# Kernel tuning notes

Hardware: AMD Instinct MI355X
Metric: run time of the kernel (lower is better)

The kernel has to match this reference:

```python
import jax, jax.numpy as jnp
import numpy as np

NT, NS, NH, NG = 365, 1024, 64, 32
NW = NH * 8 + 2


def setup_inputs() -> dict:
    key = jax.random.key(0)
    k1, k2, k3, k4 = jax.random.split(key, 4)
    std = 1.0 / np.sqrt(NH)
    x = jax.random.normal(k1, (NT, NS, 4), dtype=jnp.float32)
    # make P (precip) nonnegative and T1 < T2 plausible-ish; math is still generic
    xc = jax.random.normal(k2, (NS, NG), dtype=jnp.float32)
    fc_w = jax.random.uniform(k3, (NW, NG), minval=-std, maxval=std, dtype=jnp.float32)
    fc_b = jax.random.uniform(k4, (NW,), minval=-std, maxval=std, dtype=jnp.float32)
    return {"x": x, "xc": xc, "fc_w": fc_w, "fc_b": fc_b}


def reference(x, xc, fc_w, fc_b):
    nh = NH
    P, E, T1, T2 = x[..., 0], x[..., 1], x[..., 2], x[..., 3]  # each [nt, ns]
    Ta = (T1 + T2) * 0.5
    # rain/snow partition: rP = 1 - arccos((T1+T2)/(T2-T1))/3.1415, masked
    valid = (T1 < 0) & (T2 > 0)
    denom = jnp.where(valid, T2 - T1, 1.0)
    ratio = jnp.clip(jnp.where(valid, (T1 + T2) / denom, 0.0), -0.999999, 0.999999)
    rP = 1.0 - jnp.arccos(ratio) / 3.1415
    rP = jnp.where(T1 >= 0, 1.0, rP)
    rP = jnp.where(T2 <= 0, 0.0, rP)
    Ps = (1.0 - rP) * P  # snow   [nt, ns]
    Pl = rP * P          # liquid [nt, ns]

    w = xc @ fc_w.T + fc_b  # [ns, nh*8+2]
    gm = jnp.exp(w[:, :nh]) + 1.0
    ge = jax.nn.sigmoid(w[:, nh:2 * nh]) * 2.0
    go = jax.nn.sigmoid(w[:, 2 * nh:3 * nh])
    gl = jnp.exp(w[:, 3 * nh:4 * nh] * 2.0)
    ga = jax.nn.softmax(w[:, 4 * nh:5 * nh], axis=1)  # Dropout in eval mode = identity
    gb = jax.nn.sigmoid(w[:, 5 * nh:6 * nh])
    qb = jax.nn.relu(w[:, -1]) / nh  # [ns]
    kb = jax.nn.sigmoid(w[:, 6 * nh:7 * nh]) / 10.0
    gi = jax.nn.sigmoid(w[:, 7 * nh:8 * nh])

    ns = P.shape[1]
    init = (jnp.zeros((ns, nh), jnp.float32),) * 3  # S0, H0, G0

    def step(carry, inp):
        S0, H0, G0 = carry
        Ps_k, Pl_k, Ta_k, E_k = inp  # each [ns]
        S = S0 + Ps_k[:, None]
        Sm = jnp.minimum(S0, jax.nn.relu(Ta_k[:, None] * gm))  # snowmelt
        H = jax.nn.relu(H0 + Sm + Pl_k[:, None] * gi - E_k[:, None] * ge)
        Q1 = jax.nn.relu(H - gl)
        Q2a = jnp.minimum(H, gl) * go
        Q2 = Q2a * (1.0 - gb)
        G = G0 + Q2a * gb
        Q3 = G * kb
        H0n = jnp.minimum(H - Q2a, gl)
        G0n = G - Q3
        S0n = S - Sm
        Y = jnp.sum((Q1 + Q2 + Q3 + qb[:, None]) * ga, axis=1)  # [ns]
        return (S0n, H0n, G0n), Y

    _, Yout = jax.lax.scan(step, init, (Ps, Pl, Ta, E))
    return Yout  # [nt, ns]
```

## Files before the change

### kernel.cpp

```cpp
#include <hip/hip_runtime.h>
#include <math.h>

#define NT_ 365
#define NS_ 1024
#define NH_ 64
#define NG_ 32
#define NW_ 514
#define CH_ 64
#define NCHUNK_ 6
#define YPAD_ 65
#define SUB_ 8

__device__ __forceinline__ float sigmoidf(float v) {
  return 1.0f / (1.0f + expf(-v));
}

__device__ __forceinline__ float4 compute_met(float4 xv) {
  const float P = xv.x, E = xv.y, T1 = xv.z, T2 = xv.w;
  const float Ta = (T1 + T2) * 0.5f;
  float rP;
  if (T2 <= 0.0f) {
    rP = 0.0f;
  } else if (T1 >= 0.0f) {
    rP = 1.0f;
  } else {
    float r = (T1 + T2) / (T2 - T1);
    r = fminf(fmaxf(r, -0.999999f), 0.999999f);
    rP = 1.0f - acosf(r) * (1.0f / 3.1415f);
  }
  float4 m;
  m.x = (1.0f - rP) * P;
  m.y = rP * P;
  m.z = fmaxf(Ta, 0.0f);
  m.w = E;
  return m;
}

__global__ __launch_bounds__(256) void waternet_scan(
    const float* __restrict__ x,
    const float* __restrict__ xc,
    const float* __restrict__ fc_w,
    const float* __restrict__ fc_b,
    float* __restrict__ out)
{
  __shared__ float4 smet[4][CH_];
  __shared__ float  ytile[4][CH_ * YPAD_];

  const int tid  = threadIdx.x;
  const int lane = tid & 63;
  const int wv   = tid >> 6;
  const int site = (blockIdx.x << 2) + wv;
  const int us   = __builtin_amdgcn_readfirstlane(site);
  const float4* xp = (const float4*)x;

  float4 xcur = xp[lane * NS_ + site];

  float acc[8];
#pragma unroll
  for (int k = 0; k < 8; ++k) acc[k] = fc_b[k * NH_ + lane];
  float accq = fc_b[NW_ - 1];

  const float4* xcq = (const float4*)(xc + us * NG_);
  const float4* wq4 = (const float4*)fc_w;
#pragma unroll
  for (int g4 = 0; g4 < NG_ / 4; ++g4) {
    const float4 xv = xcq[g4];
#pragma unroll
    for (int k = 0; k < 8; ++k) {
      const float4 w = wq4[(k * NH_ + lane) * (NG_ / 4) + g4];
      acc[k] = fmaf(xv.x, w.x, acc[k]);
      acc[k] = fmaf(xv.y, w.y, acc[k]);
      acc[k] = fmaf(xv.z, w.z, acc[k]);
      acc[k] = fmaf(xv.w, w.w, acc[k]);
    }
    {
      const float4 w = wq4[(NW_ - 1) * (NG_ / 4) + g4];
      accq = fmaf(xv.x, w.x, accq);
      accq = fmaf(xv.y, w.y, accq);
      accq = fmaf(xv.z, w.z, accq);
      accq = fmaf(xv.w, w.w, accq);
    }
  }

  const float gm = expf(acc[0]) + 1.0f;
  const float ge = sigmoidf(acc[1]) * 2.0f;
  const float go = sigmoidf(acc[2]);
  const float gl = expf(acc[3] * 2.0f);
  float mx = acc[4];
#pragma unroll
  for (int mm = 32; mm >= 1; mm >>= 1) mx = fmaxf(mx, __shfl_xor(mx, mm, 64));
  const float ex = expf(acc[4] - mx);
  float sm = ex;
#pragma unroll
  for (int mm = 32; mm >= 1; mm >>= 1) sm += __shfl_xor(sm, mm, 64);
  const float ga = ex / sm;
  const float gb = sigmoidf(acc[5]);
  const float kb = sigmoidf(acc[6]) * 0.1f;
  const float gi = sigmoidf(acc[7]);
  const float qb = fmaxf(accq, 0.0f) * (1.0f / NH_);
  const float kb1m = 1.0f - kb;
  const float nge  = -ge;
  const float gq1  = go * (1.0f - gb) - 1.0f;

  float S0 = 0.0f, H0 = 0.0f, G0 = 0.0f;

  smet[wv][lane] = compute_met(xcur);

  auto step = [&](const float4 mt, float* ywaddr) {
    const float melt = mt.z * gm;
    const float Sm   = fminf(S0, melt);
    const float base = H0 + Sm;
    S0 = (S0 - Sm) + mt.x;
    const float t3 = fmaf(mt.y, gi, base);
    const float H  = fmaxf(fmaf(mt.w, nge, t3), 0.0f);
    const float M  = fminf(H, gl);
    const float Q2a = M * go;
    H0 = fminf(H - Q2a, gl);
    const float G = fmaf(Q2a, gb, G0);
    G0 = G * kb1m;
    *ywaddr = fmaf(G, kb, fmaf(M, gq1, H)) * ga;
  };

  float*       yw = &ytile[wv][lane];
  const float* yr = &ytile[wv][lane * YPAD_];

#pragma unroll 1
  for (int c = 0; c < NCHUNK_; ++c) {
    int tn = (c + 1) * CH_ + lane;
    tn = (tn < NT_) ? tn : (NT_ - 1);
    const float4 xnext = xp[tn * NS_ + site];

    const float4* mp = &smet[wv][0];

    float4 mb0[SUB_], mb1[SUB_];
#pragma unroll
    for (int u = 0; u < SUB_; ++u) mb0[u] = mp[u];

#pragma unroll
    for (int sc = 0; sc < CH_ / SUB_; ++sc) {
      float4*       cur = (sc & 1) ? mb1 : mb0;
      float4*       nxt = (sc & 1) ? mb0 : mb1;
      if (sc < CH_ / SUB_ - 1) {
#pragma unroll
        for (int u = 0; u < SUB_; ++u) nxt[u] = mp[SUB_ * (sc + 1) + u];
      }
#pragma unroll
      for (int u = 0; u < SUB_; ++u)
        step(cur[u], yw + (SUB_ * sc + u) * YPAD_);
    }

    float r0 = 0.0f, r1 = 0.0f, r2 = 0.0f, r3 = 0.0f;
#pragma unroll
    for (int h = 0; h < CH_; h += 4) {
      r0 += yr[h + 0];
      r1 += yr[h + 1];
      r2 += yr[h + 2];
      r3 += yr[h + 3];
    }
    const int t_out = c * CH_ + lane;
    if (t_out < NT_) out[t_out * NS_ + site] = ((r0 + r1) + (r2 + r3)) + qb;

    if (c + 1 < NCHUNK_) smet[wv][lane] = compute_met(xnext);
  }
}

extern "C" void kernel_launch(void* const* d_in, const int* in_sizes, int n_in,
                              void* d_out, int out_size, void* d_ws, size_t ws_size,
                              hipStream_t stream) {
  const float* x    = (const float*)d_in[0];
  const float* xc   = (const float*)d_in[1];
  const float* fc_w = (const float*)d_in[2];
  const float* fc_b = (const float*)d_in[3];
  float* out = (float*)d_out;

  hipLaunchKernelGGL(waternet_scan, dim3(NS_ / 4), dim3(256), 0, stream,
                     x, xc, fc_w, fc_b, out);
}
```

Before: 88.32 us.

## Split each site's time scan across four waves with redundant state replay

Each block now handles one site instead of four, and its four waves each own a 96-step time segment. To get the carried state at its segment start, every wave replays the recurrence from t=0 without emitting outputs, which trades redundant serial work for shorter per-wave critical paths and four times as many blocks. All meteorological inputs for the site are staged in shared memory up front behind a block barrier, and the output reduction uses 16-step chunks with vectorized LDS reads. The last wave still does roughly 288 replay steps plus 80 output steps, so the critical path may not shrink much while the total ALU work grows.

Measured after the change: 146.2 us. +65.6%, slower.

```diff
diff --git a/kernel.cpp b/kernel.cpp
--- a/kernel.cpp
+++ b/kernel.cpp
@@ -6,10 +6,10 @@
 #define NH_ 64
 #define NG_ 32
 #define NW_ 514
-#define CH_ 64
-#define NCHUNK_ 6
-#define YPAD_ 65
-#define SUB_ 8
+#define SEG_ 96
+#define CH_ 16
+#define YPAD_ 68
+#define NTPAD_ 384
 
 __device__ __forceinline__ float sigmoidf(float v) {
   return 1.0f / (1.0f + expf(-v));
@@ -36,31 +36,33 @@
   return m;
 }
 
-__global__ __launch_bounds__(256) void waternet_scan(
+__global__ __launch_bounds__(256, 4) void waternet_scan(
     const float* __restrict__ x,
     const float* __restrict__ xc,
     const float* __restrict__ fc_w,
     const float* __restrict__ fc_b,
     float* __restrict__ out)
 {
-  __shared__ float4 smet[4][CH_];
+  __shared__ float4 smet[NTPAD_];
   __shared__ float  ytile[4][CH_ * YPAD_];
 
   const int tid  = threadIdx.x;
   const int lane = tid & 63;
   const int wv   = tid >> 6;
-  const int site = (blockIdx.x << 2) + wv;
-  const int us   = __builtin_amdgcn_readfirstlane(site);
+  const int site = blockIdx.x;
   const float4* xp = (const float4*)x;
 
-  float4 xcur = xp[lane * NS_ + site];
+  const float4 xv1 = xp[tid * NS_ + site];
+  const int    t2  = 256 + tid;
+  float4 xv2 = make_float4(0.0f, 0.0f, 0.0f, 0.0f);
+  if (t2 < NT_) xv2 = xp[t2 * NS_ + site];
 
   float acc[8];
 #pragma unroll
   for (int k = 0; k < 8; ++k) acc[k] = fc_b[k * NH_ + lane];
   float accq = fc_b[NW_ - 1];
 
-  const float4* xcq = (const float4*)(xc + us * NG_);
+  const float4* xcq = (const float4*)(xc + site * NG_);
   const float4* wq4 = (const float4*)fc_w;
 #pragma unroll
   for (int g4 = 0; g4 < NG_ / 4; ++g4) {
@@ -102,65 +104,73 @@
   const float nge  = -ge;
   const float gq1  = go * (1.0f - gb) - 1.0f;
 
+  smet[tid] = compute_met(xv1);
+  if (t2 < NTPAD_) {
+    float4 m2 = make_float4(0.0f, 0.0f, 0.0f, 0.0f);
+    if (t2 < NT_) m2 = compute_met(xv2);
+    smet[t2] = m2;
+  }
+  __syncthreads();
+
   float S0 = 0.0f, H0 = 0.0f, G0 = 0.0f;
 
-  smet[wv][lane] = compute_met(xcur);
+  const int lim = wv * SEG_;
+  for (int t0 = 0; t0 < lim; t0 += 8) {
+    float4 mb[8];
+#pragma unroll
+    for (int u = 0; u < 8; ++u) mb[u] = smet[t0 + u];
+#pragma unroll
+    for (int u = 0; u < 8; ++u) {
+      const float4 mt = mb[u];
+      const float melt = mt.z * gm;
+      const float Sm   = fminf(S0, melt);
+      const float base = H0 + Sm;
+      S0 = (S0 - Sm) + mt.x;
+      const float H = fmaxf(fmaf(mt.w, nge, fmaf(mt.y, gi, base)), 0.0f);
+      const float M = fminf(H, gl);
+      const float Q2a = M * go;
+      H0 = fminf(H - Q2a, gl);
+      G0 = fmaf(Q2a, gb, G0) * kb1m;
+    }
+  }
 
-  auto step = [&](const float4 mt, float* ywaddr) {
-    const float melt = mt.z * gm;
-    const float Sm   = fminf(S0, melt);
-    const float base = H0 + Sm;
-    S0 = (S0 - Sm) + mt.x;
-    const float t3 = fmaf(mt.y, gi, base);
-    const float H  = fmaxf(fmaf(mt.w, nge, t3), 0.0f);
-    const float M  = fminf(H, gl);
-    const float Q2a = M * go;
-    H0 = fminf(H - Q2a, gl);
-    const float G = fmaf(Q2a, gb, G0);
-    G0 = G * kb1m;
-    *ywaddr = fmaf(G, kb, fmaf(M, gq1, H)) * ga;
-  };
-
+  const int segbase = lim;
+  const int nch = (wv == 3) ? 5 : 6;
   float*       yw = &ytile[wv][lane];
   const float* yr = &ytile[wv][lane * YPAD_];
 
-#pragma unroll 1
-  for (int c = 0; c < NCHUNK_; ++c) {
-    int tn = (c + 1) * CH_ + lane;
-    tn = (tn < NT_) ? tn : (NT_ - 1);
-    const float4 xnext = xp[tn * NS_ + site];
-
-    const float4* mp = &smet[wv][0];
-
-    float4 mb0[SUB_], mb1[SUB_];
+  for (int cc = 0; cc < nch; ++cc) {
+    const float4* mp = &smet[segbase + cc * CH_];
 #pragma unroll
-    for (int u = 0; u < SUB_; ++u) mb0[u] = mp[u];
-
+    for (int j = 0; j < CH_; ++j) {
+      const float4 mt = mp[j];
+      const float melt = mt.z * gm;
+      const float Sm   = fminf(S0, melt);
+      const float base = H0 + Sm;
+      S0 = (S0 - Sm) + mt.x;
+      const float H = fmaxf(fmaf(mt.w, nge, fmaf(mt.y, gi, base)), 0.0f);
+      const float M = fminf(H, gl);
+      const float Q2a = M * go;
+      H0 = fminf(H - Q2a, gl);
+      const float G = fmaf(Q2a, gb, G0);
+      G0 = G * kb1m;
+      yw[j * YPAD_] = fmaf(G, kb, fmaf(M, gq1, H)) * ga;
+    }
+    if (lane < CH_) {
+      const float4* yv = (const float4*)yr;
+      float4 r0 = yv[0], r1 = yv[1], r2 = yv[2], r3 = yv[3];
 #pragma unroll
-    for (int sc = 0; sc < CH_ / SUB_; ++sc) {
-      float4*       cur = (sc & 1) ? mb1 : mb0;
-      float4*       nxt = (sc & 1) ? mb0 : mb1;
-      if (sc < CH_ / SUB_ - 1) {
-#pragma unroll
-        for (int u = 0; u < SUB_; ++u) nxt[u] = mp[SUB_ * (sc + 1) + u];
+      for (int h = 4; h < 16; h += 4) {
+        r0 += yv[h + 0];
+        r1 += yv[h + 1];
+        r2 += yv[h + 2];
+        r3 += yv[h + 3];
       }
-#pragma unroll
-      for (int u = 0; u < SUB_; ++u)
-        step(cur[u], yw + (SUB_ * sc + u) * YPAD_);
+      const float4 rs = (r0 + r1) + (r2 + r3);
+      const float tot = (rs.x + rs.y) + (rs.z + rs.w);
+      const int t_out = segbase + cc * CH_ + lane;
+      if (t_out < NT_) out[t_out * NS_ + site] = tot + qb;
     }
-
-    float r0 = 0.0f, r1 = 0.0f, r2 = 0.0f, r3 = 0.0f;
-#pragma unroll
-    for (int h = 0; h < CH_; h += 4) {
-      r0 += yr[h + 0];
-      r1 += yr[h + 1];
-      r2 += yr[h + 2];
-      r3 += yr[h + 3];
-    }
-    const int t_out = c * CH_ + lane;
-    if (t_out < NT_) out[t_out * NS_ + site] = ((r0 + r1) + (r2 + r3)) + qb;
-
-    if (c + 1 < NCHUNK_) smet[wv][lane] = compute_met(xnext);
   }
 }
 
@@ -173,6 +183,6 @@
   const float* fc_b = (const float*)d_in[3];
   float* out = (float*)d_out;
 
-  hipLaunchKernelGGL(waternet_scan, dim3(NS_ / 4), dim3(256), 0, stream,
+  hipLaunchKernelGGL(waternet_scan, dim3(NS_), dim3(256), 0, stream,
                      x, xc, fc_w, fc_b, out);
 }
```
